# Performance work log

Hardware: AMD Instinct MI355X
Metric: run time of the kernel (lower is better)

The kernel has to match this reference:

```python
import jax, jax.numpy as jnp
import numpy as np

NEG_BIG = -9e15  # matches torch's -9000000000000000.0 mask value


def _l2norm(x, eps=1e-12):
    # F.normalize(x, p=2, dim=1)
    n = jnp.sqrt(jnp.sum(x * x, axis=1, keepdims=True))
    return x / jnp.maximum(n, eps)


def _fusion_attribute(emb, att_emb, adj):
    # cosine similarity [N, M]
    sim = _l2norm(emb) @ _l2norm(att_emb).T
    sim = sim * adj
    # masked softmax over dim=1: zeros -> -9e15
    logits = jnp.where(sim != 0, sim, jnp.full_like(sim, NEG_BIG))
    attention = jax.nn.softmax(logits, axis=1)
    return attention @ att_emb


def setup_inputs() -> dict:
    key = jax.random.key(0)
    k1, k2, k3, k4 = jax.random.split(key, 4)
    U, I, D = 10000, 8000, 64
    users_emb = 0.1 * jax.random.normal(k1, (U, D), dtype=jnp.float32)  # init.normal_(std=0.1)
    items_emb = 0.1 * jax.random.normal(k2, (I, D), dtype=jnp.float32)
    Out_UserAttNets = (jax.random.uniform(k3, (U, I)) < 0.05).astype(jnp.float32)
    Out_ItemAttNets = (jax.random.uniform(k4, (I, U)) < 0.05).astype(jnp.float32)
    return {
        "num_users": U,
        "num_items": I,
        "users_emb": users_emb,
        "items_emb": items_emb,
        "Out_UserAttNets": Out_UserAttNets,
        "Out_ItemAttNets": Out_ItemAttNets,
    }


def reference(num_users, num_items, users_emb, items_emb, Out_UserAttNets, Out_ItemAttNets):
    out_useratt_emb = _fusion_attribute(users_emb, items_emb, Out_UserAttNets)
    out_itematt_emb = _fusion_attribute(items_emb, users_emb, Out_ItemAttNets)
    return (users_emb, items_emb, out_useratt_emb, out_itematt_emb)
```

## Files before the change

kernel.cpp:

```cpp
#include <hip/hip_runtime.h>
#include <math.h>

typedef float f32x4 __attribute__((ext_vector_type(4)));
typedef unsigned int u32;
typedef u32 u32x2 __attribute__((ext_vector_type(2)));
typedef unsigned short u16;

#define SEGCAP 768

__device__ __forceinline__ u16 f2b(float x) {
    union { float f; u32 u; } v; v.f = x;
    return (u16)((v.u + 0x7FFFu + ((v.u >> 16) & 1u)) >> 16);
}
__device__ __forceinline__ float b2f_lo(u32 u) { union { u32 u; float f; } v; v.u = u << 16;         return v.f; }
__device__ __forceinline__ float b2f_hi(u32 u) { union { u32 u; float f; } v; v.u = u & 0xFFFF0000u; return v.f; }

__global__ __launch_bounds__(256) void prep_kernel(
    const float* __restrict__ users, const float* __restrict__ items,
    u16* __restrict__ hU, u16* __restrict__ hI,
    float* __restrict__ nU, float* __restrict__ nI, int U, int I)
{
    int lane = threadIdx.x & 63;
    int row  = (blockIdx.x << 2) + (threadIdx.x >> 6);
    const float* src; u16* hat; float* nrm; int r;
    if (row < U) { r = row; src = users; hat = hU; nrm = nU; }
    else { r = row - U; if (r >= I) return; src = items; hat = hI; nrm = nI; }
    float x = src[(size_t)r * 64 + lane];
    float s = x * x;
#pragma unroll
    for (int off = 32; off; off >>= 1) s += __shfl_xor(s, off, 64);
    float nv   = sqrtf(s);
    float rinv = 1.0f / fmaxf(nv, 1e-12f);
    hat[(size_t)r * 64 + lane] = f2b(x * rinv);
    if (lane == 0) nrm[r] = nv;
}

__global__ __launch_bounds__(256) void att_row_kernel(
    const float* __restrict__ users, const float* __restrict__ items,
    const u16* __restrict__ hU, const u16* __restrict__ hI,
    const float* __restrict__ nU, const float* __restrict__ nI,
    const float* __restrict__ adjU, const float* __restrict__ adjI,
    float* __restrict__ outU, float* __restrict__ outI, int U, int I)
{
    __shared__ int cols_sh[4][SEGCAP];

    const int lane = threadIdx.x & 63;
    const int wid  = threadIdx.x >> 6;
    const int grow = (blockIdx.x << 2) + wid;
    if (grow >= U + I) return;

    const u16* qhat; const u16* kvhat; const float* kvnrm;
    const float* kvraw; const float* adj; float* outp;
    int M, row;
    if (grow < U) {
        row = grow;     qhat = hU; kvhat = hI; kvnrm = nI;
        kvraw = items;  adj = adjU; outp = outU; M = I;
    } else {
        row = grow - U; qhat = hI; kvhat = hU; kvnrm = nU;
        kvraw = users;  adj = adjI; outp = outI; M = U;
    }
    const float* adjrow = adj + (size_t)row * M;

    int wcount = 0;
    const int M4 = M >> 2;
    const unsigned long long lt = (1ULL << lane) - 1ULL;
    for (int i4 = lane; i4 < M4; i4 += 64) {
        f32x4 a = __builtin_nontemporal_load((const f32x4*)adjrow + i4);
#pragma unroll
        for (int j = 0; j < 4; ++j) {
            bool pred = (a[j] != 0.0f);
            unsigned long long mask = __ballot(pred);
            if (pred) {
                int pos = wcount + __popcll(mask & lt);
                if (pos < SEGCAP) cols_sh[wid][pos] = (i4 << 2) + j;
            }
            wcount += __popcll(mask);
        }
    }
    wcount = __shfl(wcount, 0, 64);
    if (M & 3) {
        int idx = (M4 << 2) + lane;
        bool pred = (idx < M) && (adjrow[idx] != 0.0f);
        unsigned long long mask = __ballot(pred);
        if (pred) {
            int pos = wcount + __popcll(mask & lt);
            if (pos < SEGCAP) cols_sh[wid][pos] = idx;
        }
        wcount += __popcll(mask);
    }
    int cnt = wcount > SEGCAP ? SEGCAP : wcount;

    const int sub = lane & 15;
    const int grp = lane >> 4;

    u32x2 qw = *(const u32x2*)(qhat + (size_t)row * 64 + sub * 4);
    const float q0 = b2f_lo(qw[0]), q1 = b2f_hi(qw[0]);
    const float q2 = b2f_lo(qw[1]), q3 = b2f_hi(qw[1]);

    float a0 = 0.f, a1 = 0.f, a2 = 0.f, a3 = 0.f, wsum = 0.f;
    const int* cp = cols_sh[wid];

    int i = grp;
    for (; i + 12 < cnt; i += 16) {
        int c0 = cp[i], c1 = cp[i + 4], c2 = cp[i + 8], c3 = cp[i + 12];
        u32x2 v0 = *(const u32x2*)(kvhat + (size_t)c0 * 64 + sub * 4);
        u32x2 v1 = *(const u32x2*)(kvhat + (size_t)c1 * 64 + sub * 4);
        u32x2 v2 = *(const u32x2*)(kvhat + (size_t)c2 * 64 + sub * 4);
        u32x2 v3 = *(const u32x2*)(kvhat + (size_t)c3 * 64 + sub * 4);
        float n0 = kvnrm[c0], n1 = kvnrm[c1], n2 = kvnrm[c2], n3 = kvnrm[c3];
        float r00 = b2f_lo(v0[0]), r01 = b2f_hi(v0[0]), r02 = b2f_lo(v0[1]), r03 = b2f_hi(v0[1]);
        float r10 = b2f_lo(v1[0]), r11 = b2f_hi(v1[0]), r12 = b2f_lo(v1[1]), r13 = b2f_hi(v1[1]);
        float r20 = b2f_lo(v2[0]), r21 = b2f_hi(v2[0]), r22 = b2f_lo(v2[1]), r23 = b2f_hi(v2[1]);
        float r30 = b2f_lo(v3[0]), r31 = b2f_hi(v3[0]), r32 = b2f_lo(v3[1]), r33 = b2f_hi(v3[1]);
        float d0 = fmaf(q0, r00, fmaf(q1, r01, fmaf(q2, r02, q3 * r03)));
        float d1 = fmaf(q0, r10, fmaf(q1, r11, fmaf(q2, r12, q3 * r13)));
        float d2 = fmaf(q0, r20, fmaf(q1, r21, fmaf(q2, r22, q3 * r23)));
        float d3 = fmaf(q0, r30, fmaf(q1, r31, fmaf(q2, r32, q3 * r33)));
#pragma unroll
        for (int off = 1; off <= 8; off <<= 1) {
            d0 += __shfl_xor(d0, off, 64);
            d1 += __shfl_xor(d1, off, 64);
            d2 += __shfl_xor(d2, off, 64);
            d3 += __shfl_xor(d3, off, 64);
        }
        float w0 = (d0 != 0.0f) ? __expf(d0 - 1.0f) : 0.0f;
        float w1 = (d1 != 0.0f) ? __expf(d1 - 1.0f) : 0.0f;
        float w2 = (d2 != 0.0f) ? __expf(d2 - 1.0f) : 0.0f;
        float w3 = (d3 != 0.0f) ? __expf(d3 - 1.0f) : 0.0f;
        float x0 = w0 * n0, x1 = w1 * n1, x2 = w2 * n2, x3 = w3 * n3;
        a0 = fmaf(x0, r00, fmaf(x1, r10, fmaf(x2, r20, fmaf(x3, r30, a0))));
        a1 = fmaf(x0, r01, fmaf(x1, r11, fmaf(x2, r21, fmaf(x3, r31, a1))));
        a2 = fmaf(x0, r02, fmaf(x1, r12, fmaf(x2, r22, fmaf(x3, r32, a2))));
        a3 = fmaf(x0, r03, fmaf(x1, r13, fmaf(x2, r23, fmaf(x3, r33, a3))));
        if (sub == 0) wsum += (w0 + w1) + (w2 + w3);
    }
    for (; i < cnt; i += 4) {
        int c0 = cp[i];
        u32x2 v0 = *(const u32x2*)(kvhat + (size_t)c0 * 64 + sub * 4);
        float n0 = kvnrm[c0];
        float r00 = b2f_lo(v0[0]), r01 = b2f_hi(v0[0]), r02 = b2f_lo(v0[1]), r03 = b2f_hi(v0[1]);
        float d0 = fmaf(q0, r00, fmaf(q1, r01, fmaf(q2, r02, q3 * r03)));
#pragma unroll
        for (int off = 1; off <= 8; off <<= 1) d0 += __shfl_xor(d0, off, 64);
        float w0 = (d0 != 0.0f) ? __expf(d0 - 1.0f) : 0.0f;
        float x0 = w0 * n0;
        a0 = fmaf(x0, r00, a0);
        a1 = fmaf(x0, r01, a1);
        a2 = fmaf(x0, r02, a2);
        a3 = fmaf(x0, r03, a3);
        if (sub == 0) wsum += w0;
    }

#pragma unroll
    for (int off = 16; off <= 32; off <<= 1) {
        wsum += __shfl_xor(wsum, off, 64);
        a0 += __shfl_xor(a0, off, 64);
        a1 += __shfl_xor(a1, off, 64);
        a2 += __shfl_xor(a2, off, 64);
        a3 += __shfl_xor(a3, off, 64);
    }
    float den = __shfl(wsum, 0, 64);

    if (lane < 16) {
        float* orow = outp + (size_t)row * 64;
        if (den > 0.0f) {
            float inv = 1.0f / den;
            f32x4 o = (f32x4){a0 * inv, a1 * inv, a2 * inv, a3 * inv};
            ((f32x4*)orow)[lane] = o;
        } else {
            f32x4 m = (f32x4){0.f, 0.f, 0.f, 0.f};
            for (int r = 0; r < M; ++r)
                m += ((const f32x4*)(kvraw + (size_t)r * 64))[lane];
            ((f32x4*)orow)[lane] = m * (1.0f / (float)M);
        }
    }
}

extern "C" void kernel_launch(void* const* d_in, const int* in_sizes, int n_in,
                              void* d_out, int out_size, void* d_ws, size_t ws_size,
                              hipStream_t stream) {
    const float* users = (const float*)d_in[2];
    const float* items = (const float*)d_in[3];
    const float* adjU  = (const float*)d_in[4];
    const float* adjI  = (const float*)d_in[5];
    const int U = in_sizes[2] / 64;
    const int I = in_sizes[3] / 64;

    char* w = (char*)d_ws;
    u16* hU = (u16*)w;    w += (size_t)U * 64 * sizeof(u16);
    u16* hI = (u16*)w;    w += (size_t)I * 64 * sizeof(u16);
    float* nU = (float*)w; w += (size_t)U * sizeof(float);
    float* nI = (float*)w;

    float* out = (float*)d_out;

    hipMemcpyAsync(out, users, (size_t)U * 64 * sizeof(float),
                   hipMemcpyDeviceToDevice, stream);
    hipMemcpyAsync(out + (size_t)U * 64, items, (size_t)I * 64 * sizeof(float),
                   hipMemcpyDeviceToDevice, stream);

    prep_kernel<<<(U + I + 3) / 4, 256, 0, stream>>>(users, items, hU, hI, nU, nI, U, I);

    float* outUatt = out + (size_t)(U + I) * 64;
    float* outIatt = outUatt + (size_t)U * 64;
    att_row_kernel<<<(U + I + 3) / 4, 256, 0, stream>>>(
        users, items, hU, hI, nU, nI, adjU, adjI, outUatt, outIatt, U, I);
}
```

Measured before the change: 220.5 us.

## Persistent waves overlap next-row adjacency scan with current-row gather

Turns the attention kernel into a persistent grid of at most 1024 blocks, where each wave steps through rows with a grid stride. Within one loop the wave scans the next row's adjacency mask into a double-buffered shared column list while it gathers and accumulates the current row's neighbours. The aim is to hide the latency of the large streaming adjacency read behind the gather and exp work. The cost is more control logic, higher register pressure with launch_bounds removed, and fewer resident waves to cover memory latency.

```diff
diff --git a/kernel.cpp b/kernel.cpp
--- a/kernel.cpp
+++ b/kernel.cpp
@@ -5,6 +5,7 @@
 typedef unsigned int u32;
 typedef u32 u32x2 __attribute__((ext_vector_type(2)));
 typedef unsigned short u16;
+typedef unsigned long long u64;
 
 #define SEGCAP 768
 
@@ -35,144 +36,187 @@
     if (lane == 0) nrm[r] = nv;
 }
 
-__global__ __launch_bounds__(256) void att_row_kernel(
+__global__ void att_row_kernel(
     const float* __restrict__ users, const float* __restrict__ items,
     const u16* __restrict__ hU, const u16* __restrict__ hI,
     const float* __restrict__ nU, const float* __restrict__ nI,
     const float* __restrict__ adjU, const float* __restrict__ adjI,
-    float* __restrict__ outU, float* __restrict__ outI, int U, int I)
+    float* __restrict__ outU, float* __restrict__ outI,
+    int U, int I, int NWAVES)
 {
-    __shared__ int cols_sh[4][SEGCAP];
+    __shared__ int cols_sh[4][2][SEGCAP];
 
     const int lane = threadIdx.x & 63;
     const int wid  = threadIdx.x >> 6;
-    const int grow = (blockIdx.x << 2) + wid;
-    if (grow >= U + I) return;
-
-    const u16* qhat; const u16* kvhat; const float* kvnrm;
-    const float* kvraw; const float* adj; float* outp;
-    int M, row;
-    if (grow < U) {
-        row = grow;     qhat = hU; kvhat = hI; kvnrm = nI;
-        kvraw = items;  adj = adjU; outp = outU; M = I;
-    } else {
-        row = grow - U; qhat = hI; kvhat = hU; kvnrm = nU;
-        kvraw = users;  adj = adjI; outp = outI; M = U;
-    }
-    const float* adjrow = adj + (size_t)row * M;
-
-    int wcount = 0;
-    const int M4 = M >> 2;
-    const unsigned long long lt = (1ULL << lane) - 1ULL;
-    for (int i4 = lane; i4 < M4; i4 += 64) {
-        f32x4 a = __builtin_nontemporal_load((const f32x4*)adjrow + i4);
-#pragma unroll
-        for (int j = 0; j < 4; ++j) {
-            bool pred = (a[j] != 0.0f);
-            unsigned long long mask = __ballot(pred);
-            if (pred) {
-                int pos = wcount + __popcll(mask & lt);
-                if (pos < SEGCAP) cols_sh[wid][pos] = (i4 << 2) + j;
-            }
-            wcount += __popcll(mask);
-        }
-    }
-    wcount = __shfl(wcount, 0, 64);
-    if (M & 3) {
-        int idx = (M4 << 2) + lane;
-        bool pred = (idx < M) && (adjrow[idx] != 0.0f);
-        unsigned long long mask = __ballot(pred);
-        if (pred) {
-            int pos = wcount + __popcll(mask & lt);
-            if (pos < SEGCAP) cols_sh[wid][pos] = idx;
-        }
-        wcount += __popcll(mask);
-    }
-    int cnt = wcount > SEGCAP ? SEGCAP : wcount;
+    const int gw   = ((int)blockIdx.x << 2) + wid;
+    const int TOT  = U + I;
 
     const int sub = lane & 15;
     const int grp = lane >> 4;
-
-    u32x2 qw = *(const u32x2*)(qhat + (size_t)row * 64 + sub * 4);
-    const float q0 = b2f_lo(qw[0]), q1 = b2f_hi(qw[0]);
-    const float q2 = b2f_lo(qw[1]), q3 = b2f_hi(qw[1]);
-
-    float a0 = 0.f, a1 = 0.f, a2 = 0.f, a3 = 0.f, wsum = 0.f;
-    const int* cp = cols_sh[wid];
-
-    int i = grp;
-    for (; i + 12 < cnt; i += 16) {
-        int c0 = cp[i], c1 = cp[i + 4], c2 = cp[i + 8], c3 = cp[i + 12];
-        u32x2 v0 = *(const u32x2*)(kvhat + (size_t)c0 * 64 + sub * 4);
-        u32x2 v1 = *(const u32x2*)(kvhat + (size_t)c1 * 64 + sub * 4);
-        u32x2 v2 = *(const u32x2*)(kvhat + (size_t)c2 * 64 + sub * 4);
-        u32x2 v3 = *(const u32x2*)(kvhat + (size_t)c3 * 64 + sub * 4);
-        float n0 = kvnrm[c0], n1 = kvnrm[c1], n2 = kvnrm[c2], n3 = kvnrm[c3];
-        float r00 = b2f_lo(v0[0]), r01 = b2f_hi(v0[0]), r02 = b2f_lo(v0[1]), r03 = b2f_hi(v0[1]);
-        float r10 = b2f_lo(v1[0]), r11 = b2f_hi(v1[0]), r12 = b2f_lo(v1[1]), r13 = b2f_hi(v1[1]);
-        float r20 = b2f_lo(v2[0]), r21 = b2f_hi(v2[0]), r22 = b2f_lo(v2[1]), r23 = b2f_hi(v2[1]);
-        float r30 = b2f_lo(v3[0]), r31 = b2f_hi(v3[0]), r32 = b2f_lo(v3[1]), r33 = b2f_hi(v3[1]);
-        float d0 = fmaf(q0, r00, fmaf(q1, r01, fmaf(q2, r02, q3 * r03)));
-        float d1 = fmaf(q0, r10, fmaf(q1, r11, fmaf(q2, r12, q3 * r13)));
-        float d2 = fmaf(q0, r20, fmaf(q1, r21, fmaf(q2, r22, q3 * r23)));
-        float d3 = fmaf(q0, r30, fmaf(q1, r31, fmaf(q2, r32, q3 * r33)));
-#pragma unroll
-        for (int off = 1; off <= 8; off <<= 1) {
-            d0 += __shfl_xor(d0, off, 64);
-            d1 += __shfl_xor(d1, off, 64);
-            d2 += __shfl_xor(d2, off, 64);
-            d3 += __shfl_xor(d3, off, 64);
-        }
-        float w0 = (d0 != 0.0f) ? __expf(d0 - 1.0f) : 0.0f;
-        float w1 = (d1 != 0.0f) ? __expf(d1 - 1.0f) : 0.0f;
-        float w2 = (d2 != 0.0f) ? __expf(d2 - 1.0f) : 0.0f;
-        float w3 = (d3 != 0.0f) ? __expf(d3 - 1.0f) : 0.0f;
-        float x0 = w0 * n0, x1 = w1 * n1, x2 = w2 * n2, x3 = w3 * n3;
-        a0 = fmaf(x0, r00, fmaf(x1, r10, fmaf(x2, r20, fmaf(x3, r30, a0))));
-        a1 = fmaf(x0, r01, fmaf(x1, r11, fmaf(x2, r21, fmaf(x3, r31, a1))));
-        a2 = fmaf(x0, r02, fmaf(x1, r12, fmaf(x2, r22, fmaf(x3, r32, a2))));
-        a3 = fmaf(x0, r03, fmaf(x1, r13, fmaf(x2, r23, fmaf(x3, r33, a3))));
-        if (sub == 0) wsum += (w0 + w1) + (w2 + w3);
-    }
-    for (; i < cnt; i += 4) {
-        int c0 = cp[i];
-        u32x2 v0 = *(const u32x2*)(kvhat + (size_t)c0 * 64 + sub * 4);
-        float n0 = kvnrm[c0];
-        float r00 = b2f_lo(v0[0]), r01 = b2f_hi(v0[0]), r02 = b2f_lo(v0[1]), r03 = b2f_hi(v0[1]);
-        float d0 = fmaf(q0, r00, fmaf(q1, r01, fmaf(q2, r02, q3 * r03)));
-#pragma unroll
-        for (int off = 1; off <= 8; off <<= 1) d0 += __shfl_xor(d0, off, 64);
-        float w0 = (d0 != 0.0f) ? __expf(d0 - 1.0f) : 0.0f;
-        float x0 = w0 * n0;
-        a0 = fmaf(x0, r00, a0);
-        a1 = fmaf(x0, r01, a1);
-        a2 = fmaf(x0, r02, a2);
-        a3 = fmaf(x0, r03, a3);
-        if (sub == 0) wsum += w0;
-    }
-
-#pragma unroll
-    for (int off = 16; off <= 32; off <<= 1) {
-        wsum += __shfl_xor(wsum, off, 64);
-        a0 += __shfl_xor(a0, off, 64);
-        a1 += __shfl_xor(a1, off, 64);
-        a2 += __shfl_xor(a2, off, 64);
-        a3 += __shfl_xor(a3, off, 64);
-    }
-    float den = __shfl(wsum, 0, 64);
-
-    if (lane < 16) {
-        float* orow = outp + (size_t)row * 64;
-        if (den > 0.0f) {
-            float inv = 1.0f / den;
-            f32x4 o = (f32x4){a0 * inv, a1 * inv, a2 * inv, a3 * inv};
-            ((f32x4*)orow)[lane] = o;
+    const u64 lt  = (1ULL << lane) - 1ULL;
+
+    int row_ok = 0, rloc_c = 0, M_c = 0, cnt_cur = 0;
+    const u16* kvhat_c = 0; const float* kvnrm_c = 0; const float* kvraw_c = 0;
+    float* outp_c = 0;
+    float q0 = 0.f, q1 = 0.f, q2 = 0.f, q3 = 0.f;
+    int p = 0;
+
+    int row_next = gw;
+    while (row_next < TOT || row_ok) {
+        const bool have_next = (row_next < TOT);
+        const float* adjrow_n = 0;
+        int M_n = 0, M4_n = 0, JC = 0, rloc_n = 0;
+        const u16 *qhat_n = 0, *kvhat_n = 0;
+        const float *kvnrm_n = 0, *kvraw_n = 0;
+        float* outp_n = 0;
+        if (have_next) {
+            if (row_next < U) {
+                rloc_n = row_next;     qhat_n = hU; kvhat_n = hI; kvnrm_n = nI;
+                kvraw_n = items; outp_n = outU; M_n = I;
+                adjrow_n = adjU + (size_t)rloc_n * M_n;
+            } else {
+                rloc_n = row_next - U; qhat_n = hI; kvhat_n = hU; kvnrm_n = nU;
+                kvraw_n = users; outp_n = outI; M_n = U;
+                adjrow_n = adjI + (size_t)rloc_n * M_n;
+            }
+            M4_n = M_n >> 2;
+            JC = (M4_n + 63) >> 6;
+        }
+        const int JG = (cnt_cur > 12) ? ((cnt_cur + 3) >> 4) : 0;
+        const int Jmax = JC > JG ? JC : JG;
+
+        int wcount = 0;
+        int ci = lane;
+        f32x4 a_cur = (f32x4){0.f, 0.f, 0.f, 0.f};
+        if (have_next && ci < M4_n)
+            a_cur = __builtin_nontemporal_load((const f32x4*)adjrow_n + ci);
+
+        float a0 = 0.f, a1 = 0.f, a2 = 0.f, a3 = 0.f, wsum = 0.f;
+        int gi = grp;
+        const int* cp = cols_sh[wid][p];
+        int* cw = cols_sh[wid][p ^ 1];
+
+        for (int j = 0; j < Jmax; ++j) {
+            if (j < JC) {
+                const int ci_nxt = ci + 64;
+                f32x4 a_nxt = (f32x4){0.f, 0.f, 0.f, 0.f};
+                if (ci_nxt < M4_n)
+                    a_nxt = __builtin_nontemporal_load((const f32x4*)adjrow_n + ci_nxt);
+#pragma unroll
+                for (int jj = 0; jj < 4; ++jj) {
+                    bool pred = (a_cur[jj] != 0.0f);
+                    u64 mask = __ballot(pred);
+                    if (pred) {
+                        int pos = wcount + __popcll(mask & lt);
+                        if (pos < SEGCAP) cw[pos] = (ci << 2) + jj;
+                    }
+                    wcount += __popcll(mask);
+                }
+                a_cur = a_nxt;
+                ci = ci_nxt;
+            }
+            if (gi + 12 < cnt_cur) {
+                int c0 = cp[gi], c1 = cp[gi + 4], c2 = cp[gi + 8], c3 = cp[gi + 12];
+                u32x2 v0 = *(const u32x2*)(kvhat_c + (size_t)c0 * 64 + sub * 4);
+                u32x2 v1 = *(const u32x2*)(kvhat_c + (size_t)c1 * 64 + sub * 4);
+                u32x2 v2 = *(const u32x2*)(kvhat_c + (size_t)c2 * 64 + sub * 4);
+                u32x2 v3 = *(const u32x2*)(kvhat_c + (size_t)c3 * 64 + sub * 4);
+                float n0 = kvnrm_c[c0], n1 = kvnrm_c[c1], n2 = kvnrm_c[c2], n3 = kvnrm_c[c3];
+                float r00 = b2f_lo(v0[0]), r01 = b2f_hi(v0[0]), r02 = b2f_lo(v0[1]), r03 = b2f_hi(v0[1]);
+                float r10 = b2f_lo(v1[0]), r11 = b2f_hi(v1[0]), r12 = b2f_lo(v1[1]), r13 = b2f_hi(v1[1]);
+                float r20 = b2f_lo(v2[0]), r21 = b2f_hi(v2[0]), r22 = b2f_lo(v2[1]), r23 = b2f_hi(v2[1]);
+                float r30 = b2f_lo(v3[0]), r31 = b2f_hi(v3[0]), r32 = b2f_lo(v3[1]), r33 = b2f_hi(v3[1]);
+                float d0 = fmaf(q0, r00, fmaf(q1, r01, fmaf(q2, r02, q3 * r03)));
+                float d1 = fmaf(q0, r10, fmaf(q1, r11, fmaf(q2, r12, q3 * r13)));
+                float d2 = fmaf(q0, r20, fmaf(q1, r21, fmaf(q2, r22, q3 * r23)));
+                float d3 = fmaf(q0, r30, fmaf(q1, r31, fmaf(q2, r32, q3 * r33)));
+#pragma unroll
+                for (int off = 1; off <= 8; off <<= 1) {
+                    d0 += __shfl_xor(d0, off, 64);
+                    d1 += __shfl_xor(d1, off, 64);
+                    d2 += __shfl_xor(d2, off, 64);
+                    d3 += __shfl_xor(d3, off, 64);
+                }
+                float w0 = (d0 != 0.0f) ? __expf(d0 - 1.0f) : 0.0f;
+                float w1 = (d1 != 0.0f) ? __expf(d1 - 1.0f) : 0.0f;
+                float w2 = (d2 != 0.0f) ? __expf(d2 - 1.0f) : 0.0f;
+                float w3 = (d3 != 0.0f) ? __expf(d3 - 1.0f) : 0.0f;
+                float x0 = w0 * n0, x1 = w1 * n1, x2 = w2 * n2, x3 = w3 * n3;
+                a0 = fmaf(x0, r00, fmaf(x1, r10, fmaf(x2, r20, fmaf(x3, r30, a0))));
+                a1 = fmaf(x0, r01, fmaf(x1, r11, fmaf(x2, r21, fmaf(x3, r31, a1))));
+                a2 = fmaf(x0, r02, fmaf(x1, r12, fmaf(x2, r22, fmaf(x3, r32, a2))));
+                a3 = fmaf(x0, r03, fmaf(x1, r13, fmaf(x2, r23, fmaf(x3, r33, a3))));
+                if (sub == 0) wsum += (w0 + w1) + (w2 + w3);
+                gi += 16;
+            }
+        }
+        int cnt_next = 0;
+        if (have_next) {
+            int wc = __shfl(wcount, 0, 64);
+            if (M_n & 3) {
+                int idx = (M4_n << 2) + lane;
+                bool pred = (idx < M_n) && (adjrow_n[idx] != 0.0f);
+                u64 mask = __ballot(pred);
+                if (pred) {
+                    int pos = wc + __popcll(mask & lt);
+                    if (pos < SEGCAP) cw[pos] = idx;
+                }
+                wc += __popcll(mask);
+            }
+            cnt_next = wc > SEGCAP ? SEGCAP : wc;
+        }
+        if (row_ok) {
+            for (; gi < cnt_cur; gi += 4) {
+                int c0 = cp[gi];
+                u32x2 v0 = *(const u32x2*)(kvhat_c + (size_t)c0 * 64 + sub * 4);
+                float n0 = kvnrm_c[c0];
+                float r00 = b2f_lo(v0[0]), r01 = b2f_hi(v0[0]), r02 = b2f_lo(v0[1]), r03 = b2f_hi(v0[1]);
+                float d0 = fmaf(q0, r00, fmaf(q1, r01, fmaf(q2, r02, q3 * r03)));
+#pragma unroll
+                for (int off = 1; off <= 8; off <<= 1) d0 += __shfl_xor(d0, off, 64);
+                float w0 = (d0 != 0.0f) ? __expf(d0 - 1.0f) : 0.0f;
+                float x0 = w0 * n0;
+                a0 = fmaf(x0, r00, a0);
+                a1 = fmaf(x0, r01, a1);
+                a2 = fmaf(x0, r02, a2);
+                a3 = fmaf(x0, r03, a3);
+                if (sub == 0) wsum += w0;
+            }
+#pragma unroll
+            for (int off = 16; off <= 32; off <<= 1) {
+                wsum += __shfl_xor(wsum, off, 64);
+                a0 += __shfl_xor(a0, off, 64);
+                a1 += __shfl_xor(a1, off, 64);
+                a2 += __shfl_xor(a2, off, 64);
+                a3 += __shfl_xor(a3, off, 64);
+            }
+            float den = __shfl(wsum, 0, 64);
+            if (lane < 16) {
+                float* orow = outp_c + (size_t)rloc_c * 64;
+                if (den > 0.0f) {
+                    float inv = 1.0f / den;
+                    ((f32x4*)orow)[lane] = (f32x4){a0 * inv, a1 * inv, a2 * inv, a3 * inv};
+                } else {
+                    f32x4 m = (f32x4){0.f, 0.f, 0.f, 0.f};
+                    for (int r = 0; r < M_c; ++r)
+                        m += ((const f32x4*)(kvraw_c + (size_t)r * 64))[lane];
+                    ((f32x4*)orow)[lane] = m * (1.0f / (float)M_c);
+                }
+            }
+        }
+        if (have_next) {
+            row_ok = 1;
+            rloc_c = rloc_n; M_c = M_n; cnt_cur = cnt_next;
+            kvhat_c = kvhat_n; kvnrm_c = kvnrm_n; kvraw_c = kvraw_n; outp_c = outp_n;
+            u32x2 qw = *(const u32x2*)(qhat_n + (size_t)rloc_n * 64 + sub * 4);
+            q0 = b2f_lo(qw[0]); q1 = b2f_hi(qw[0]);
+            q2 = b2f_lo(qw[1]); q3 = b2f_hi(qw[1]);
+            p ^= 1;
         } else {
-            f32x4 m = (f32x4){0.f, 0.f, 0.f, 0.f};
-            for (int r = 0; r < M; ++r)
-                m += ((const f32x4*)(kvraw + (size_t)r * 64))[lane];
-            ((f32x4*)orow)[lane] = m * (1.0f / (float)M);
-        }
+            row_ok = 0;
+            cnt_cur = 0;
+        }
+        row_next += NWAVES;
     }
 }
 
@@ -203,6 +247,9 @@
 
     float* outUatt = out + (size_t)(U + I) * 64;
     float* outIatt = outUatt + (size_t)U * 64;
-    att_row_kernel<<<(U + I + 3) / 4, 256, 0, stream>>>(
-        users, items, hU, hI, nU, nI, adjU, adjI, outUatt, outIatt, U, I);
-}
+
+    int G = (U + I + 3) / 4;
+    if (G > 1024) G = 1024;
+    att_row_kernel<<<G, 256, 0, stream>>>(
+        users, items, hU, hI, nU, nI, adjU, adjI, outUatt, outIatt, U, I, G * 4);
+}
```

New measurement: 275.7 us. 25.1% more time.

## Use persistent grid-stride waves and 8-lane-per-row gathers with 16-byte loads

Applied to the files above, without the earlier changes.

The attention kernel becomes a persistent grid-stride loop capped at 2048 blocks. Each wave now walks many rows instead of launching one wave per row. The gather phase switches from 16 lanes × 8 bytes to 8 lanes × 16 bytes per key row, so each wave handles 8 keys per step with fewer shuffle reduction steps. Lane prefix counts now use mbcnt intrinsics. The aim is to cut launch and tail overhead and per-key shuffle cost, at the price of more registers per lane and less overlap between rows within a wave.

```diff
diff --git a/kernel.cpp b/kernel.cpp
--- a/kernel.cpp
+++ b/kernel.cpp
@@ -3,8 +3,9 @@
 
 typedef float f32x4 __attribute__((ext_vector_type(4)));
 typedef unsigned int u32;
-typedef u32 u32x2 __attribute__((ext_vector_type(2)));
+typedef u32 u32x4 __attribute__((ext_vector_type(4)));
 typedef unsigned short u16;
+typedef unsigned long long u64;
 
 #define SEGCAP 768
 
@@ -40,138 +41,149 @@
     const u16* __restrict__ hU, const u16* __restrict__ hI,
     const float* __restrict__ nU, const float* __restrict__ nI,
     const float* __restrict__ adjU, const float* __restrict__ adjI,
-    float* __restrict__ outU, float* __restrict__ outI, int U, int I)
+    float* __restrict__ outU, float* __restrict__ outI,
+    int U, int I, int NWAVES)
 {
     __shared__ int cols_sh[4][SEGCAP];
 
     const int lane = threadIdx.x & 63;
     const int wid  = threadIdx.x >> 6;
-    const int grow = (blockIdx.x << 2) + wid;
-    if (grow >= U + I) return;
-
-    const u16* qhat; const u16* kvhat; const float* kvnrm;
-    const float* kvraw; const float* adj; float* outp;
-    int M, row;
-    if (grow < U) {
-        row = grow;     qhat = hU; kvhat = hI; kvnrm = nI;
-        kvraw = items;  adj = adjU; outp = outU; M = I;
-    } else {
-        row = grow - U; qhat = hI; kvhat = hU; kvnrm = nU;
-        kvraw = users;  adj = adjI; outp = outI; M = U;
-    }
-    const float* adjrow = adj + (size_t)row * M;
-
-    int wcount = 0;
-    const int M4 = M >> 2;
-    const unsigned long long lt = (1ULL << lane) - 1ULL;
-    for (int i4 = lane; i4 < M4; i4 += 64) {
-        f32x4 a = __builtin_nontemporal_load((const f32x4*)adjrow + i4);
-#pragma unroll
-        for (int j = 0; j < 4; ++j) {
-            bool pred = (a[j] != 0.0f);
-            unsigned long long mask = __ballot(pred);
+    const int TOT  = U + I;
+
+    const int sub = lane & 7;
+    const int grp = lane >> 3;
+
+    for (int grow = ((int)blockIdx.x << 2) + wid; grow < TOT; grow += NWAVES) {
+        const u16* qhat; const u16* kvhat; const float* kvnrm;
+        const float* kvraw; const float* adj; float* outp;
+        int M, row;
+        if (grow < U) {
+            row = grow;     qhat = hU; kvhat = hI; kvnrm = nI;
+            kvraw = items;  adj = adjU; outp = outU; M = I;
+        } else {
+            row = grow - U; qhat = hI; kvhat = hU; kvnrm = nU;
+            kvraw = users;  adj = adjI; outp = outI; M = U;
+        }
+        const float* adjrow = adj + (size_t)row * M;
+
+        int wcount = 0;
+        const int M4 = M >> 2;
+        for (int i4 = lane; i4 < M4; i4 += 64) {
+            f32x4 a = __builtin_nontemporal_load((const f32x4*)adjrow + i4);
+#pragma unroll
+            for (int j = 0; j < 4; ++j) {
+                bool pred = (a[j] != 0.0f);
+                u64 mask = __ballot(pred);
+                if (pred) {
+                    int pos = wcount + __builtin_amdgcn_mbcnt_hi(
+                        (u32)(mask >> 32), __builtin_amdgcn_mbcnt_lo((u32)mask, 0));
+                    if (pos < SEGCAP) cols_sh[wid][pos] = (i4 << 2) + j;
+                }
+                wcount += __popcll(mask);
+            }
+        }
+        wcount = __shfl(wcount, 0, 64);
+        if (M & 3) {
+            int idx = (M4 << 2) + lane;
+            bool pred = (idx < M) && (adjrow[idx] != 0.0f);
+            u64 mask = __ballot(pred);
             if (pred) {
-                int pos = wcount + __popcll(mask & lt);
-                if (pos < SEGCAP) cols_sh[wid][pos] = (i4 << 2) + j;
+                int pos = wcount + __builtin_amdgcn_mbcnt_hi(
+                    (u32)(mask >> 32), __builtin_amdgcn_mbcnt_lo((u32)mask, 0));
+                if (pos < SEGCAP) cols_sh[wid][pos] = idx;
             }
             wcount += __popcll(mask);
         }
-    }
-    wcount = __shfl(wcount, 0, 64);
-    if (M & 3) {
-        int idx = (M4 << 2) + lane;
-        bool pred = (idx < M) && (adjrow[idx] != 0.0f);
-        unsigned long long mask = __ballot(pred);
-        if (pred) {
-            int pos = wcount + __popcll(mask & lt);
-            if (pos < SEGCAP) cols_sh[wid][pos] = idx;
-        }
-        wcount += __popcll(mask);
-    }
-    int cnt = wcount > SEGCAP ? SEGCAP : wcount;
-
-    const int sub = lane & 15;
-    const int grp = lane >> 4;
-
-    u32x2 qw = *(const u32x2*)(qhat + (size_t)row * 64 + sub * 4);
-    const float q0 = b2f_lo(qw[0]), q1 = b2f_hi(qw[0]);
-    const float q2 = b2f_lo(qw[1]), q3 = b2f_hi(qw[1]);
-
-    float a0 = 0.f, a1 = 0.f, a2 = 0.f, a3 = 0.f, wsum = 0.f;
-    const int* cp = cols_sh[wid];
-
-    int i = grp;
-    for (; i + 12 < cnt; i += 16) {
-        int c0 = cp[i], c1 = cp[i + 4], c2 = cp[i + 8], c3 = cp[i + 12];
-        u32x2 v0 = *(const u32x2*)(kvhat + (size_t)c0 * 64 + sub * 4);
-        u32x2 v1 = *(const u32x2*)(kvhat + (size_t)c1 * 64 + sub * 4);
-        u32x2 v2 = *(const u32x2*)(kvhat + (size_t)c2 * 64 + sub * 4);
-        u32x2 v3 = *(const u32x2*)(kvhat + (size_t)c3 * 64 + sub * 4);
-        float n0 = kvnrm[c0], n1 = kvnrm[c1], n2 = kvnrm[c2], n3 = kvnrm[c3];
-        float r00 = b2f_lo(v0[0]), r01 = b2f_hi(v0[0]), r02 = b2f_lo(v0[1]), r03 = b2f_hi(v0[1]);
-        float r10 = b2f_lo(v1[0]), r11 = b2f_hi(v1[0]), r12 = b2f_lo(v1[1]), r13 = b2f_hi(v1[1]);
-        float r20 = b2f_lo(v2[0]), r21 = b2f_hi(v2[0]), r22 = b2f_lo(v2[1]), r23 = b2f_hi(v2[1]);
-        float r30 = b2f_lo(v3[0]), r31 = b2f_hi(v3[0]), r32 = b2f_lo(v3[1]), r33 = b2f_hi(v3[1]);
-        float d0 = fmaf(q0, r00, fmaf(q1, r01, fmaf(q2, r02, q3 * r03)));
-        float d1 = fmaf(q0, r10, fmaf(q1, r11, fmaf(q2, r12, q3 * r13)));
-        float d2 = fmaf(q0, r20, fmaf(q1, r21, fmaf(q2, r22, q3 * r23)));
-        float d3 = fmaf(q0, r30, fmaf(q1, r31, fmaf(q2, r32, q3 * r33)));
-#pragma unroll
-        for (int off = 1; off <= 8; off <<= 1) {
-            d0 += __shfl_xor(d0, off, 64);
-            d1 += __shfl_xor(d1, off, 64);
-            d2 += __shfl_xor(d2, off, 64);
-            d3 += __shfl_xor(d3, off, 64);
-        }
-        float w0 = (d0 != 0.0f) ? __expf(d0 - 1.0f) : 0.0f;
-        float w1 = (d1 != 0.0f) ? __expf(d1 - 1.0f) : 0.0f;
-        float w2 = (d2 != 0.0f) ? __expf(d2 - 1.0f) : 0.0f;
-        float w3 = (d3 != 0.0f) ? __expf(d3 - 1.0f) : 0.0f;
-        float x0 = w0 * n0, x1 = w1 * n1, x2 = w2 * n2, x3 = w3 * n3;
-        a0 = fmaf(x0, r00, fmaf(x1, r10, fmaf(x2, r20, fmaf(x3, r30, a0))));
-        a1 = fmaf(x0, r01, fmaf(x1, r11, fmaf(x2, r21, fmaf(x3, r31, a1))));
-        a2 = fmaf(x0, r02, fmaf(x1, r12, fmaf(x2, r22, fmaf(x3, r32, a2))));
-        a3 = fmaf(x0, r03, fmaf(x1, r13, fmaf(x2, r23, fmaf(x3, r33, a3))));
-        if (sub == 0) wsum += (w0 + w1) + (w2 + w3);
-    }
-    for (; i < cnt; i += 4) {
-        int c0 = cp[i];
-        u32x2 v0 = *(const u32x2*)(kvhat + (size_t)c0 * 64 + sub * 4);
-        float n0 = kvnrm[c0];
-        float r00 = b2f_lo(v0[0]), r01 = b2f_hi(v0[0]), r02 = b2f_lo(v0[1]), r03 = b2f_hi(v0[1]);
-        float d0 = fmaf(q0, r00, fmaf(q1, r01, fmaf(q2, r02, q3 * r03)));
-#pragma unroll
-        for (int off = 1; off <= 8; off <<= 1) d0 += __shfl_xor(d0, off, 64);
-        float w0 = (d0 != 0.0f) ? __expf(d0 - 1.0f) : 0.0f;
-        float x0 = w0 * n0;
-        a0 = fmaf(x0, r00, a0);
-        a1 = fmaf(x0, r01, a1);
-        a2 = fmaf(x0, r02, a2);
-        a3 = fmaf(x0, r03, a3);
-        if (sub == 0) wsum += w0;
-    }
-
-#pragma unroll
-    for (int off = 16; off <= 32; off <<= 1) {
-        wsum += __shfl_xor(wsum, off, 64);
-        a0 += __shfl_xor(a0, off, 64);
-        a1 += __shfl_xor(a1, off, 64);
-        a2 += __shfl_xor(a2, off, 64);
-        a3 += __shfl_xor(a3, off, 64);
-    }
-    float den = __shfl(wsum, 0, 64);
-
-    if (lane < 16) {
-        float* orow = outp + (size_t)row * 64;
-        if (den > 0.0f) {
-            float inv = 1.0f / den;
-            f32x4 o = (f32x4){a0 * inv, a1 * inv, a2 * inv, a3 * inv};
-            ((f32x4*)orow)[lane] = o;
-        } else {
-            f32x4 m = (f32x4){0.f, 0.f, 0.f, 0.f};
-            for (int r = 0; r < M; ++r)
-                m += ((const f32x4*)(kvraw + (size_t)r * 64))[lane];
-            ((f32x4*)orow)[lane] = m * (1.0f / (float)M);
+        int cnt = wcount > SEGCAP ? SEGCAP : wcount;
+
+        u32x4 qw = *(const u32x4*)(qhat + (size_t)row * 64 + sub * 8);
+        const float q0 = b2f_lo(qw[0]), q1 = b2f_hi(qw[0]);
+        const float q2 = b2f_lo(qw[1]), q3 = b2f_hi(qw[1]);
+        const float q4 = b2f_lo(qw[2]), q5 = b2f_hi(qw[2]);
+        const float q6 = b2f_lo(qw[3]), q7 = b2f_hi(qw[3]);
+
+        float a0 = 0.f, a1 = 0.f, a2 = 0.f, a3 = 0.f;
+        float a4 = 0.f, a5 = 0.f, a6 = 0.f, a7 = 0.f, wsum = 0.f;
+        const int* cp = cols_sh[wid];
+
+        int i = grp;
+        for (; i + 8 < cnt; i += 16) {
+            int ca = cp[i], cb = cp[i + 8];
+            u32x4 va = *(const u32x4*)(kvhat + (size_t)ca * 64 + sub * 8);
+            u32x4 vb = *(const u32x4*)(kvhat + (size_t)cb * 64 + sub * 8);
+            float na = kvnrm[ca], nb = kvnrm[cb];
+            float ra0 = b2f_lo(va[0]), ra1 = b2f_hi(va[0]), ra2 = b2f_lo(va[1]), ra3 = b2f_hi(va[1]);
+            float ra4 = b2f_lo(va[2]), ra5 = b2f_hi(va[2]), ra6 = b2f_lo(va[3]), ra7 = b2f_hi(va[3]);
+            float rb0 = b2f_lo(vb[0]), rb1 = b2f_hi(vb[0]), rb2 = b2f_lo(vb[1]), rb3 = b2f_hi(vb[1]);
+            float rb4 = b2f_lo(vb[2]), rb5 = b2f_hi(vb[2]), rb6 = b2f_lo(vb[3]), rb7 = b2f_hi(vb[3]);
+            float da = fmaf(q0, ra0, fmaf(q1, ra1, fmaf(q2, ra2, fmaf(q3, ra3,
+                       fmaf(q4, ra4, fmaf(q5, ra5, fmaf(q6, ra6, q7 * ra7)))))));
+            float db = fmaf(q0, rb0, fmaf(q1, rb1, fmaf(q2, rb2, fmaf(q3, rb3,
+                       fmaf(q4, rb4, fmaf(q5, rb5, fmaf(q6, rb6, q7 * rb7)))))));
+#pragma unroll
+            for (int off = 1; off <= 4; off <<= 1) {
+                da += __shfl_xor(da, off, 64);
+                db += __shfl_xor(db, off, 64);
+            }
+            float wa = (da != 0.0f) ? __expf(da - 1.0f) : 0.0f;
+            float wb = (db != 0.0f) ? __expf(db - 1.0f) : 0.0f;
+            float xa = wa * na, xb = wb * nb;
+            a0 = fmaf(xa, ra0, fmaf(xb, rb0, a0));
+            a1 = fmaf(xa, ra1, fmaf(xb, rb1, a1));
+            a2 = fmaf(xa, ra2, fmaf(xb, rb2, a2));
+            a3 = fmaf(xa, ra3, fmaf(xb, rb3, a3));
+            a4 = fmaf(xa, ra4, fmaf(xb, rb4, a4));
+            a5 = fmaf(xa, ra5, fmaf(xb, rb5, a5));
+            a6 = fmaf(xa, ra6, fmaf(xb, rb6, a6));
+            a7 = fmaf(xa, ra7, fmaf(xb, rb7, a7));
+            if (sub == 0) wsum += wa + wb;
+        }
+        for (; i < cnt; i += 8) {
+            int ca = cp[i];
+            u32x4 va = *(const u32x4*)(kvhat + (size_t)ca * 64 + sub * 8);
+            float na = kvnrm[ca];
+            float ra0 = b2f_lo(va[0]), ra1 = b2f_hi(va[0]), ra2 = b2f_lo(va[1]), ra3 = b2f_hi(va[1]);
+            float ra4 = b2f_lo(va[2]), ra5 = b2f_hi(va[2]), ra6 = b2f_lo(va[3]), ra7 = b2f_hi(va[3]);
+            float da = fmaf(q0, ra0, fmaf(q1, ra1, fmaf(q2, ra2, fmaf(q3, ra3,
+                       fmaf(q4, ra4, fmaf(q5, ra5, fmaf(q6, ra6, q7 * ra7)))))));
+#pragma unroll
+            for (int off = 1; off <= 4; off <<= 1) da += __shfl_xor(da, off, 64);
+            float wa = (da != 0.0f) ? __expf(da - 1.0f) : 0.0f;
+            float xa = wa * na;
+            a0 = fmaf(xa, ra0, a0); a1 = fmaf(xa, ra1, a1);
+            a2 = fmaf(xa, ra2, a2); a3 = fmaf(xa, ra3, a3);
+            a4 = fmaf(xa, ra4, a4); a5 = fmaf(xa, ra5, a5);
+            a6 = fmaf(xa, ra6, a6); a7 = fmaf(xa, ra7, a7);
+            if (sub == 0) wsum += wa;
+        }
+
+#pragma unroll
+        for (int off = 8; off <= 32; off <<= 1) {
+            wsum += __shfl_xor(wsum, off, 64);
+            a0 += __shfl_xor(a0, off, 64); a1 += __shfl_xor(a1, off, 64);
+            a2 += __shfl_xor(a2, off, 64); a3 += __shfl_xor(a3, off, 64);
+            a4 += __shfl_xor(a4, off, 64); a5 += __shfl_xor(a5, off, 64);
+            a6 += __shfl_xor(a6, off, 64); a7 += __shfl_xor(a7, off, 64);
+        }
+        float den = __shfl(wsum, 0, 64);
+
+        if (lane < 8) {
+            float* orow = outp + (size_t)row * 64 + lane * 8;
+            if (den > 0.0f) {
+                float inv = 1.0f / den;
+                ((f32x4*)orow)[0] = (f32x4){a0 * inv, a1 * inv, a2 * inv, a3 * inv};
+                ((f32x4*)orow)[1] = (f32x4){a4 * inv, a5 * inv, a6 * inv, a7 * inv};
+            } else {
+                f32x4 m0 = (f32x4){0.f, 0.f, 0.f, 0.f};
+                f32x4 m1 = (f32x4){0.f, 0.f, 0.f, 0.f};
+                for (int r = 0; r < M; ++r) {
+                    const f32x4* kr = (const f32x4*)(kvraw + (size_t)r * 64 + lane * 8);
+                    m0 += kr[0]; m1 += kr[1];
+                }
+                float invM = 1.0f / (float)M;
+                ((f32x4*)orow)[0] = m0 * invM;
+                ((f32x4*)orow)[1] = m1 * invM;
+            }
         }
     }
 }
@@ -203,6 +215,9 @@
 
     float* outUatt = out + (size_t)(U + I) * 64;
     float* outIatt = outUatt + (size_t)U * 64;
-    att_row_kernel<<<(U + I + 3) / 4, 256, 0, stream>>>(
-        users, items, hU, hI, nU, nI, adjU, adjI, outUatt, outIatt, U, I);
-}
+
+    int G = (U + I + 3) / 4;
+    if (G > 2048) G = 2048;
+    att_row_kernel<<<G, 256, 0, stream>>>(
+        users, items, hU, hI, nU, nI, adjU, adjI, outUatt, outIatt, U, I, G * 4);
+}
```

After: 233.8 us. +6.0%, slower.
